# Performance work log

Hardware: AMD Instinct MI355X
Metric: run time of the kernel (lower is better)

Reference implementation:

```python
import jax, jax.numpy as jnp
import numpy as np

N_NODES = 50000
N_EDGES = 1600000
IN_FEAT = 128
HIDDEN = 128
CLASSES = 2


def gin_conv(x, src, dst, W, b, n_nodes):
    # GINConv (eps=0): h_i = mlp(x_i + sum_{j in N(i)} x_j)
    agg = jax.ops.segment_sum(x[src], dst, num_segments=n_nodes)  # [N, F]
    h = x + agg
    return h @ W + b


def setup_inputs() -> dict:
    key = jax.random.key(0)
    ks = jax.random.split(key, 8)
    x = jax.random.normal(ks[0], (N_NODES, IN_FEAT), dtype=jnp.float32)
    edge_index = jax.random.randint(ks[1], (2, N_EDGES), 0, N_NODES, dtype=jnp.int64)
    def lin(k, fan_in, fan_out):
        kw, kb = jax.random.split(k)
        bound = 1.0 / np.sqrt(fan_in)
        W = jax.random.uniform(kw, (fan_in, fan_out), jnp.float32, -bound, bound)
        b = jax.random.uniform(kb, (fan_out,), jnp.float32, -bound, bound)
        return W, b
    W1, b1 = lin(ks[2], IN_FEAT, HIDDEN)
    W2, b2 = lin(ks[3], HIDDEN, HIDDEN)
    W3, b3 = lin(ks[4], HIDDEN, CLASSES)
    return {"x": x, "edge_index": edge_index, "W1": W1, "b1": b1,
            "W2": W2, "b2": b2, "W3": W3, "b3": b3}


def reference(x, edge_index, W1, b1, W2, b2, W3, b3):
    src, dst = edge_index[0], edge_index[1]
    n = x.shape[0]
    h = jax.nn.relu(gin_conv(x, src, dst, W1, b1, n))
    h = jax.nn.relu(gin_conv(h, src, dst, W2, b2, n))
    return gin_conv(h, src, dst, W3, b3, n)
```

## Files before the change

### kernel.cpp

```cpp
#include <hip/hip_runtime.h>

#define NNODES 50000
#define NEDGES 1600000
#define F 128

#define NB 128
#define BSH 391
#define BCAP 13312
#define EPT 10

typedef __attribute__((ext_vector_type(8))) short bf16x8;
typedef __attribute__((ext_vector_type(4))) float f32x4;

__device__ inline unsigned short f2bf(float f) {
    union { float f; unsigned u; } v; v.f = f;
    unsigned r = v.u + 0x7FFF + ((v.u >> 16) & 1);
    return (unsigned short)(r >> 16);
}
__device__ inline float2 up2(ushort2 h) {
    union { unsigned u; float f; } a, b;
    a.u = ((unsigned)h.x) << 16; b.u = ((unsigned)h.y) << 16;
    return make_float2(a.f, b.f);
}

__global__ __launch_bounds__(256) void cvt_bf16(const float4* __restrict__ in,
                                                ushort4* __restrict__ out, int n4) {
    int i = blockIdx.x * blockDim.x + threadIdx.x;
    int stride = gridDim.x * blockDim.x;
    for (; i < n4; i += stride) {
        float4 v = in[i];
        ushort4 o;
        o.x = f2bf(v.x); o.y = f2bf(v.y); o.z = f2bf(v.z); o.w = f2bf(v.w);
        out[i] = o;
    }
}

__global__ __launch_bounds__(256) void wprep2(const float* __restrict__ W1,
                                              const float* __restrict__ W2,
                                              unsigned short* __restrict__ Wf1,
                                              unsigned short* __restrict__ Wf2) {
    int id = blockIdx.x * 256 + threadIdx.x;
    const float* W = (id < 2048) ? W1 : W2;
    unsigned short* Wf = (id < 2048) ? Wf1 : Wf2;
    id &= 2047;
    const int l = id & 63, nn = (id >> 6) & 7, s = id >> 9;
    const int c = nn * 16 + (l & 15);
    const int k0 = s * 32 + (l >> 4) * 8;
    ushort4 lo, hi;
    lo.x = f2bf(W[(k0 + 0) * F + c]); lo.y = f2bf(W[(k0 + 1) * F + c]);
    lo.z = f2bf(W[(k0 + 2) * F + c]); lo.w = f2bf(W[(k0 + 3) * F + c]);
    hi.x = f2bf(W[(k0 + 4) * F + c]); hi.y = f2bf(W[(k0 + 5) * F + c]);
    hi.z = f2bf(W[(k0 + 6) * F + c]); hi.w = f2bf(W[(k0 + 7) * F + c]);
    ushort4* p = (ushort4*)(Wf + (size_t)id * 8);
    p[0] = lo; p[1] = hi;
}

__global__ __launch_bounds__(256) void bucketA(const int* __restrict__ src,
                                               const int* __restrict__ dst,
                                               unsigned* __restrict__ E1,
                                               int* __restrict__ gcnt) {
    __shared__ unsigned hist[NB];
    __shared__ unsigned start[NB];
    const int t = threadIdx.x;
    if (t < NB) hist[t] = 0;
    __syncthreads();
    const int base = blockIdx.x * (256 * EPT);
    unsigned rec[EPT]; int bkt[EPT];
#pragma unroll
    for (int k = 0; k < EPT; ++k) {
        const int i = base + k * 256 + t;
        const int s = src[i], d = dst[i];
        const int b = d / BSH;
        rec[k] = ((unsigned)s << 9) | (unsigned)(d - b * BSH);
        bkt[k] = b;
        atomicAdd(&hist[b], 1u);
    }
    __syncthreads();
    if (t < NB) {
        unsigned h = hist[t];
        start[t] = h ? (unsigned)atomicAdd(&gcnt[t], (int)h) : 0u;
        hist[t] = 0;
    }
    __syncthreads();
#pragma unroll
    for (int k = 0; k < EPT; ++k) {
        const int b = bkt[k];
        const unsigned p = start[b] + atomicAdd(&hist[b], 1u);
        if (p < BCAP) E1[(size_t)b * BCAP + p] = rec[k];
    }
}

__global__ __launch_bounds__(64) void scanB(const int* __restrict__ gcnt,
                                            int* __restrict__ bstart,
                                            int* __restrict__ off) {
    const int lane = threadIdx.x;
    int a0 = gcnt[lane * 2], a1 = gcnt[lane * 2 + 1];
    int s = a0 + a1, inc = s;
#pragma unroll
    for (int o = 1; o <= 32; o <<= 1) {
        int u = __shfl_up(inc, o);
        if (lane >= o) inc += u;
    }
    int excl = inc - s;
    bstart[lane * 2] = excl;
    bstart[lane * 2 + 1] = excl + a0;
    if (lane == 63) off[NNODES] = NEDGES;
}

__global__ __launch_bounds__(256) void bucketB(const unsigned* __restrict__ E1,
                                               const int* __restrict__ gcnt,
                                               const int* __restrict__ bstart,
                                               int* __restrict__ off,
                                               unsigned short* __restrict__ ssrc) {
    __shared__ int cnt[BSH];
    __shared__ int cur[BSH];
    __shared__ int wtot[4];
    const int b = blockIdx.x, t = threadIdx.x;
    const int ne = min(gcnt[b], BCAP);
    const int ebase = bstart[b];
    const unsigned* E = E1 + (size_t)b * BCAP;
    for (int i = t; i < BSH; i += 256) cnt[i] = 0;
    __syncthreads();
    for (int i = t; i < ne; i += 256) atomicAdd(&cnt[E[i] & 511], 1);
    __syncthreads();
    const int i0 = t * 2, i1 = t * 2 + 1;
    const int a0 = (i0 < BSH) ? cnt[i0] : 0;
    const int a1 = (i1 < BSH) ? cnt[i1] : 0;
    const int s = a0 + a1;
    int inc = s;
    const int lane = t & 63, w = t >> 6;
#pragma unroll
    for (int o = 1; o <= 32; o <<= 1) {
        int u = __shfl_up(inc, o);
        if (lane >= o) inc += u;
    }
    if (lane == 63) wtot[w] = inc;
    __syncthreads();
    int woff = 0;
    for (int k = 0; k < w; ++k) woff += wtot[k];
    const int excl = woff + inc - s;
    if (i0 < BSH) {
        cur[i0] = excl;
        const int n = b * BSH + i0;
        if (n < NNODES) off[n] = ebase + excl;
    }
    if (i1 < BSH) {
        cur[i1] = excl + a0;
        const int n = b * BSH + i1;
        if (n < NNODES) off[n] = ebase + excl + a0;
    }
    __syncthreads();
    for (int i = t; i < ne; i += 256) {
        const unsigned rec = E[i];
        const int r = atomicAdd(&cur[rec & 511], 1);
        ssrc[ebase + r] = (unsigned short)(rec >> 9);
    }
}

__global__ __launch_bounds__(256) void agg_bf16(const ushort2* __restrict__ h,
                                                const int* __restrict__ off,
                                                const unsigned short* __restrict__ ssrc,
                                                ushort2* __restrict__ S, int n) {
    const int wid = (blockIdx.x * blockDim.x + threadIdx.x) >> 6;
    const int lane = threadIdx.x & 63;
    if (wid >= n) return;
    const int e0 = off[wid], e1 = off[wid + 1];
    float2 acc = up2(h[(size_t)wid * 64 + lane]);
    int e = e0;
    for (; e + 4 <= e1; e += 4) {
        const int s0 = ssrc[e], s1 = ssrc[e + 1], s2 = ssrc[e + 2], s3 = ssrc[e + 3];
        const float2 v0 = up2(h[(size_t)s0 * 64 + lane]);
        const float2 v1 = up2(h[(size_t)s1 * 64 + lane]);
        const float2 v2 = up2(h[(size_t)s2 * 64 + lane]);
        const float2 v3 = up2(h[(size_t)s3 * 64 + lane]);
        acc.x += v0.x + v1.x + v2.x + v3.x;
        acc.y += v0.y + v1.y + v2.y + v3.y;
    }
    for (; e < e1; ++e) {
        const float2 v = up2(h[(size_t)ssrc[e] * 64 + lane]);
        acc.x += v.x;
        acc.y += v.y;
    }
    ushort2 o;
    o.x = f2bf(acc.x); o.y = f2bf(acc.y);
    S[(size_t)wid * 64 + lane] = o;
}

__global__ __launch_bounds__(256) void mlp_mfma(const unsigned short* __restrict__ Sb,
                                                const unsigned short* __restrict__ Wfrag,
                                                const float* __restrict__ bias,
                                                unsigned short* __restrict__ Hb,
                                                int n, int relu) {
    const int wave = threadIdx.x >> 6, lane = threadIdx.x & 63;
    const int base = blockIdx.x * 64 + wave * 16;
    const int r16 = lane & 15, hi = lane >> 4;
    int arow = base + r16;
    if (arow >= n) arow = n - 1;
    const unsigned short* Arow = Sb + (size_t)arow * F;

    f32x4 acc[8];
#pragma unroll
    for (int i = 0; i < 8; ++i) acc[i] = (f32x4){0.f, 0.f, 0.f, 0.f};

#pragma unroll
    for (int s = 0; s < 4; ++s) {
        const bf16x8 a = *(const bf16x8*)(Arow + s * 32 + hi * 8);
#pragma unroll
        for (int nn = 0; nn < 8; ++nn) {
            const bf16x8 b = *(const bf16x8*)(Wfrag + ((size_t)(s * 8 + nn) * 64 + lane) * 8);
            acc[nn] = __builtin_amdgcn_mfma_f32_16x16x32_bf16(a, b, acc[nn], 0, 0, 0);
        }
    }

#pragma unroll
    for (int nn = 0; nn < 8; ++nn) {
        const int col = nn * 16 + r16;
        const float bv = bias[col];
#pragma unroll
        for (int r = 0; r < 4; ++r) {
            const int row = base + hi * 4 + r;
            if (row < n) {
                float v = acc[nn][r] + bv;
                if (relu) v = fmaxf(v, 0.f);
                Hb[(size_t)row * F + col] = f2bf(v);
            }
        }
    }
}

__global__ __launch_bounds__(256) void head_t(const ushort2* __restrict__ Hb,
                                              const float4* __restrict__ W3,
                                              float2* __restrict__ y, int n) {
    const int wid = (blockIdx.x * blockDim.x + threadIdx.x) >> 6;
    const int lane = threadIdx.x & 63;
    if (wid >= n) return;
    const float2 h = up2(Hb[(size_t)wid * 64 + lane]);
    const float4 w = W3[lane];
    float a0 = h.x * w.x + h.y * w.z;
    float a1 = h.x * w.y + h.y * w.w;
#pragma unroll
    for (int o = 32; o; o >>= 1) {
        a0 += __shfl_xor(a0, o);
        a1 += __shfl_xor(a1, o);
    }
    if (lane == 0) y[wid] = make_float2(a0, a1);
}

__global__ __launch_bounds__(256) void agg3(const float2* __restrict__ y,
                                            const int* __restrict__ off,
                                            const unsigned short* __restrict__ ssrc,
                                            const float* __restrict__ b3,
                                            float2* __restrict__ out, int n) {
    const int i = blockIdx.x * blockDim.x + threadIdx.x;
    if (i >= n) return;
    float2 acc = y[i];
    const int e1 = off[i + 1];
    for (int e = off[i]; e < e1; ++e) {
        const float2 v = y[ssrc[e]];
        acc.x += v.x;
        acc.y += v.y;
    }
    out[i] = make_float2(acc.x + b3[0], acc.y + b3[1]);
}

extern "C" void kernel_launch(void* const* d_in, const int* in_sizes, int n_in,
                              void* d_out, int out_size, void* d_ws, size_t ws_size,
                              hipStream_t stream) {
    const float* x  = (const float*)d_in[0];
    const int* ei   = (const int*)d_in[1];
    const int* src  = ei;
    const int* dst  = ei + NEDGES;
    const float* W1 = (const float*)d_in[2];
    const float* b1 = (const float*)d_in[3];
    const float* W2 = (const float*)d_in[4];
    const float* b2 = (const float*)d_in[5];
    const float* W3 = (const float*)d_in[6];
    const float* b3 = (const float*)d_in[7];
    float* out = (float*)d_out;

    char* ws = (char*)d_ws;
    const size_t featB = (size_t)NNODES * F * 2;
    unsigned short* xb = (unsigned short*)ws;
    unsigned short* Sb = (unsigned short*)(ws + featB);
    unsigned short* Hb = (unsigned short*)(ws + 2 * featB);
    char* p = ws + 3 * featB;
    float* y3 = (float*)p;                 p += (size_t)NNODES * 2 * 4 + 256;
    unsigned short* Wf1 = (unsigned short*)p; p += 2048 * 8 * 2;
    unsigned short* Wf2 = (unsigned short*)p; p += 2048 * 8 * 2;
    unsigned* E1 = (unsigned*)p;           p += (size_t)NB * BCAP * 4;
    int* gcnt = (int*)p;                   p += NB * 4;
    int* bstart = (int*)p;                 p += (NB + 1) * 4 + 256;
    int* off = (int*)p;                    p += (size_t)(NNODES + 1) * 4 + 256;
    unsigned short* ssrc = (unsigned short*)p;

    hipMemsetAsync(gcnt, 0, NB * sizeof(int), stream);
    cvt_bf16<<<1024, 256, 0, stream>>>((const float4*)x, (ushort4*)xb, NNODES * F / 4);
    wprep2<<<16, 256, 0, stream>>>(W1, W2, Wf1, Wf2);

    bucketA<<<NEDGES / (256 * EPT), 256, 0, stream>>>(src, dst, E1, gcnt);
    scanB<<<1, 64, 0, stream>>>(gcnt, bstart, off);
    bucketB<<<NB, 256, 0, stream>>>(E1, gcnt, bstart, off, ssrc);

    const int aggBlocks = (NNODES + 3) / 4;
    const int mlpBlocks = (NNODES + 63) / 64;

    agg_bf16<<<aggBlocks, 256, 0, stream>>>((const ushort2*)xb, off, ssrc, (ushort2*)Sb, NNODES);
    mlp_mfma<<<mlpBlocks, 256, 0, stream>>>(Sb, Wf1, b1, Hb, NNODES, 1);

    agg_bf16<<<aggBlocks, 256, 0, stream>>>((const ushort2*)Hb, off, ssrc, (ushort2*)Sb, NNODES);
    mlp_mfma<<<mlpBlocks, 256, 0, stream>>>(Sb, Wf2, b2, xb, NNODES, 1);

    head_t<<<aggBlocks, 256, 0, stream>>>((const ushort2*)xb, (const float4*)W3, (float2*)y3, NNODES);
    agg3<<<(NNODES + 255) / 256, 256, 0, stream>>>((const float2*)y3, off, ssrc, b3, (float2*)out, NNODES);
}
```

Before: 314.5 us.

## Fold memset and scan into neighbors, per-wave histograms, shuffle-broadcast edge indices

Drops the hipMemsetAsync and the scanB kernel: wprep2 now zeroes the bucket counters and each bucketB block recomputes the bucket prefix scan itself. bucketA keeps a separate shared histogram per wave to reduce LDS atomic contention. agg_bf16 loads 64 edge indices per wave in one coalesced read and broadcasts them with shuffles, unrolling the gather by 8. The aim is fewer launches and less per-edge index-load latency, at the cost of redundant scan work in every bucketB block.

```diff
diff --git a/kernel.cpp b/kernel.cpp
--- a/kernel.cpp
+++ b/kernel.cpp
@@ -38,8 +38,10 @@
 __global__ __launch_bounds__(256) void wprep2(const float* __restrict__ W1,
                                               const float* __restrict__ W2,
                                               unsigned short* __restrict__ Wf1,
-                                              unsigned short* __restrict__ Wf2) {
+                                              unsigned short* __restrict__ Wf2,
+                                              int* __restrict__ gcnt) {
     int id = blockIdx.x * 256 + threadIdx.x;
+    if (blockIdx.x == 0 && threadIdx.x < NB) gcnt[threadIdx.x] = 0;
     const float* W = (id < 2048) ? W1 : W2;
     unsigned short* Wf = (id < 2048) ? Wf1 : Wf2;
     id &= 2047;
@@ -59,10 +61,10 @@
                                                const int* __restrict__ dst,
                                                unsigned* __restrict__ E1,
                                                int* __restrict__ gcnt) {
-    __shared__ unsigned hist[NB];
-    __shared__ unsigned start[NB];
-    const int t = threadIdx.x;
-    if (t < NB) hist[t] = 0;
+    __shared__ unsigned hist[4][NB];
+    __shared__ unsigned start[4][NB];
+    const int t = threadIdx.x, w = t >> 6;
+    for (int i = t; i < 4 * NB; i += 256) ((unsigned*)hist)[i] = 0;
     __syncthreads();
     const int base = blockIdx.x * (256 * EPT);
     unsigned rec[EPT]; int bkt[EPT];
@@ -73,54 +75,54 @@
         const int b = d / BSH;
         rec[k] = ((unsigned)s << 9) | (unsigned)(d - b * BSH);
         bkt[k] = b;
-        atomicAdd(&hist[b], 1u);
+        atomicAdd(&hist[w][b], 1u);
     }
     __syncthreads();
     if (t < NB) {
-        unsigned h = hist[t];
-        start[t] = h ? (unsigned)atomicAdd(&gcnt[t], (int)h) : 0u;
-        hist[t] = 0;
+        const unsigned h0 = hist[0][t], h1 = hist[1][t], h2 = hist[2][t], h3 = hist[3][t];
+        const unsigned tot = h0 + h1 + h2 + h3;
+        const unsigned g = tot ? (unsigned)atomicAdd(&gcnt[t], (int)tot) : 0u;
+        start[0][t] = g;
+        start[1][t] = g + h0;
+        start[2][t] = g + h0 + h1;
+        start[3][t] = g + h0 + h1 + h2;
+        hist[0][t] = 0; hist[1][t] = 0; hist[2][t] = 0; hist[3][t] = 0;
     }
     __syncthreads();
 #pragma unroll
     for (int k = 0; k < EPT; ++k) {
         const int b = bkt[k];
-        const unsigned p = start[b] + atomicAdd(&hist[b], 1u);
+        const unsigned p = start[w][b] + atomicAdd(&hist[w][b], 1u);
         if (p < BCAP) E1[(size_t)b * BCAP + p] = rec[k];
     }
-}
-
-__global__ __launch_bounds__(64) void scanB(const int* __restrict__ gcnt,
-                                            int* __restrict__ bstart,
-                                            int* __restrict__ off) {
-    const int lane = threadIdx.x;
-    int a0 = gcnt[lane * 2], a1 = gcnt[lane * 2 + 1];
-    int s = a0 + a1, inc = s;
-#pragma unroll
-    for (int o = 1; o <= 32; o <<= 1) {
-        int u = __shfl_up(inc, o);
-        if (lane >= o) inc += u;
-    }
-    int excl = inc - s;
-    bstart[lane * 2] = excl;
-    bstart[lane * 2 + 1] = excl + a0;
-    if (lane == 63) off[NNODES] = NEDGES;
 }
 
 __global__ __launch_bounds__(256) void bucketB(const unsigned* __restrict__ E1,
                                                const int* __restrict__ gcnt,
-                                               const int* __restrict__ bstart,
                                                int* __restrict__ off,
                                                unsigned short* __restrict__ ssrc) {
     __shared__ int cnt[BSH];
     __shared__ int cur[BSH];
     __shared__ int wtot[4];
+    __shared__ int bst[NB];
     const int b = blockIdx.x, t = threadIdx.x;
+    if (t < 64) {
+        const int a0 = gcnt[t * 2], a1 = gcnt[t * 2 + 1];
+        const int s = a0 + a1;
+        int inc = s;
+#pragma unroll
+        for (int o = 1; o <= 32; o <<= 1) {
+            int u = __shfl_up(inc, o);
+            if (t >= o) inc += u;
+        }
+        bst[t * 2] = inc - s;
+        bst[t * 2 + 1] = inc - s + a0;
+    }
+    for (int i = t; i < BSH; i += 256) cnt[i] = 0;
+    __syncthreads();
     const int ne = min(gcnt[b], BCAP);
-    const int ebase = bstart[b];
+    const int ebase = bst[b];
     const unsigned* E = E1 + (size_t)b * BCAP;
-    for (int i = t; i < BSH; i += 256) cnt[i] = 0;
-    __syncthreads();
     for (int i = t; i < ne; i += 256) atomicAdd(&cnt[E[i] & 511], 1);
     __syncthreads();
     const int i0 = t * 2, i1 = t * 2 + 1;
@@ -149,6 +151,7 @@
         const int n = b * BSH + i1;
         if (n < NNODES) off[n] = ebase + excl + a0;
     }
+    if (b == NB - 1 && t == 0) off[NNODES] = NEDGES;
     __syncthreads();
     for (int i = t; i < ne; i += 256) {
         const unsigned rec = E[i];
@@ -166,20 +169,32 @@
     if (wid >= n) return;
     const int e0 = off[wid], e1 = off[wid + 1];
     float2 acc = up2(h[(size_t)wid * 64 + lane]);
-    int e = e0;
-    for (; e + 4 <= e1; e += 4) {
-        const int s0 = ssrc[e], s1 = ssrc[e + 1], s2 = ssrc[e + 2], s3 = ssrc[e + 3];
-        const float2 v0 = up2(h[(size_t)s0 * 64 + lane]);
-        const float2 v1 = up2(h[(size_t)s1 * 64 + lane]);
-        const float2 v2 = up2(h[(size_t)s2 * 64 + lane]);
-        const float2 v3 = up2(h[(size_t)s3 * 64 + lane]);
-        acc.x += v0.x + v1.x + v2.x + v3.x;
-        acc.y += v0.y + v1.y + v2.y + v3.y;
-    }
-    for (; e < e1; ++e) {
-        const float2 v = up2(h[(size_t)ssrc[e] * 64 + lane]);
-        acc.x += v.x;
-        acc.y += v.y;
+    for (int base = e0; base < e1; base += 64) {
+        const int cnt = min(64, e1 - base);
+        const int myidx = (base + lane < e1) ? (int)ssrc[base + lane] : 0;
+        int i = 0;
+        for (; i + 8 <= cnt; i += 8) {
+            const int s0 = __shfl(myidx, i + 0), s1 = __shfl(myidx, i + 1);
+            const int s2 = __shfl(myidx, i + 2), s3 = __shfl(myidx, i + 3);
+            const int s4 = __shfl(myidx, i + 4), s5 = __shfl(myidx, i + 5);
+            const int s6 = __shfl(myidx, i + 6), s7 = __shfl(myidx, i + 7);
+            const float2 v0 = up2(h[(size_t)s0 * 64 + lane]);
+            const float2 v1 = up2(h[(size_t)s1 * 64 + lane]);
+            const float2 v2 = up2(h[(size_t)s2 * 64 + lane]);
+            const float2 v3 = up2(h[(size_t)s3 * 64 + lane]);
+            const float2 v4 = up2(h[(size_t)s4 * 64 + lane]);
+            const float2 v5 = up2(h[(size_t)s5 * 64 + lane]);
+            const float2 v6 = up2(h[(size_t)s6 * 64 + lane]);
+            const float2 v7 = up2(h[(size_t)s7 * 64 + lane]);
+            acc.x += ((v0.x + v1.x) + (v2.x + v3.x)) + ((v4.x + v5.x) + (v6.x + v7.x));
+            acc.y += ((v0.y + v1.y) + (v2.y + v3.y)) + ((v4.y + v5.y) + (v6.y + v7.y));
+        }
+        for (; i < cnt; ++i) {
+            const int s = __shfl(myidx, i);
+            const float2 v = up2(h[(size_t)s * 64 + lane]);
+            acc.x += v.x;
+            acc.y += v.y;
+        }
     }
     ushort2 o;
     o.x = f2bf(acc.x); o.y = f2bf(acc.y);
@@ -288,18 +303,15 @@
     unsigned short* Wf1 = (unsigned short*)p; p += 2048 * 8 * 2;
     unsigned short* Wf2 = (unsigned short*)p; p += 2048 * 8 * 2;
     unsigned* E1 = (unsigned*)p;           p += (size_t)NB * BCAP * 4;
-    int* gcnt = (int*)p;                   p += NB * 4;
-    int* bstart = (int*)p;                 p += (NB + 1) * 4 + 256;
+    int* gcnt = (int*)p;                   p += NB * 4 + 256;
     int* off = (int*)p;                    p += (size_t)(NNODES + 1) * 4 + 256;
     unsigned short* ssrc = (unsigned short*)p;
 
-    hipMemsetAsync(gcnt, 0, NB * sizeof(int), stream);
     cvt_bf16<<<1024, 256, 0, stream>>>((const float4*)x, (ushort4*)xb, NNODES * F / 4);
-    wprep2<<<16, 256, 0, stream>>>(W1, W2, Wf1, Wf2);
+    wprep2<<<16, 256, 0, stream>>>(W1, W2, Wf1, Wf2, gcnt);
 
     bucketA<<<NEDGES / (256 * EPT), 256, 0, stream>>>(src, dst, E1, gcnt);
-    scanB<<<1, 64, 0, stream>>>(gcnt, bstart, off);
-    bucketB<<<NB, 256, 0, stream>>>(E1, gcnt, bstart, off, ssrc);
+    bucketB<<<NB, 256, 0, stream>>>(E1, gcnt, off, ssrc);
 
     const int aggBlocks = (NNODES + 3) / 4;
     const int mlpBlocks = (NNODES + 63) / 64;
```

New measurement: 291.3 us. 7.4% less time.
